# Kernel tuning notes

Measured on AMD Instinct MI355X. Metric: run time of the kernel, lower is better.

The kernel has to match this reference:

```python
import jax, jax.numpy as jnp
import numpy as np

B, CIN, COUT, H, W = 4, 128, 128, 128, 128
KH = KW = 3
KK = KH * KW
MAX_RES = 3.0


def _conv3x3(x, w, b):
    y = jax.lax.conv_general_dilated(x, w, window_strides=(1, 1), padding='SAME',
                                     dimension_numbers=('NCHW', 'OIHW', 'NCHW'))
    return y + b[None, :, None, None]


def _lrelu(x):
    return jnp.where(x >= 0, x, 0.1 * x)


def _deform_conv2d(x, offset, mask, weight, bias):
    # x: [B,C,H,W]; offset: [B,2*KK,H,W] (pairs dy,dx per tap); mask: [B,KK,H,W]
    b, c, h, w = x.shape
    cout = weight.shape[0]
    ki, kj = jnp.meshgrid(jnp.arange(KH), jnp.arange(KW), indexing='ij')
    ki = ki.reshape(KK).astype(x.dtype)
    kj = kj.reshape(KK).astype(x.dtype)
    # stride=1, padding=1, dilation=1 -> base sample position = p - 1 + k
    base_y = jnp.arange(h, dtype=x.dtype)[None, :, None] - 1.0 + ki[:, None, None]  # [KK,H,1]
    base_x = jnp.arange(w, dtype=x.dtype)[None, None, :] - 1.0 + kj[:, None, None]  # [KK,1,W]
    off = offset.reshape(b, KK, 2, h, w)
    py = base_y[None] + off[:, :, 0]  # [B,KK,H,W]
    px = base_x[None] + off[:, :, 1]
    y0 = jnp.floor(py)
    x0 = jnp.floor(px)

    def gather(img, yi, xi):  # img [C,H,W], yi/xi [KK,H,W] -> [C,KK,H,W]
        return img[:, yi, xi]

    acc = jnp.zeros((b, c, KK, h, w), dtype=x.dtype)
    for dy in (0.0, 1.0):  # 4 bilinear corners (fixed small loop)
        for dx in (0.0, 1.0):
            yc = y0 + dy
            xc = x0 + dx
            wgt = (1.0 - jnp.abs(py - yc)) * (1.0 - jnp.abs(px - xc))
            valid = (yc >= 0) & (yc <= h - 1) & (xc >= 0) & (xc <= w - 1)  # zero pad outside
            yi = jnp.clip(yc, 0, h - 1).astype(jnp.int32)
            xi = jnp.clip(xc, 0, w - 1).astype(jnp.int32)
            vals = jax.vmap(gather)(x, yi, xi)  # [B,C,KK,H,W]
            acc = acc + vals * (wgt * valid)[:, None]
    acc = acc * mask[:, None]  # modulation
    out = jnp.einsum('bckhw,ock->bohw', acc, weight.reshape(cout, c, KK))
    return out + bias[None, :, None, None]


def setup_inputs() -> dict:
    key = jax.random.key(0)
    ks = jax.random.split(key, 8)

    def he(k, shape):
        fan_in = shape[1] * shape[2] * shape[3]
        return jax.random.normal(k, shape, jnp.float32) * np.float32(np.sqrt(2.0 / fan_in))

    ccond = 2 * COUT + 2 + 1 + 2  # 261
    return {
        'x': jax.random.normal(ks[0], (B, CIN, H, W), jnp.float32),
        'cond_feat': jax.random.normal(ks[1], (B, ccond, H, W), jnp.float32),
        'flow': jax.random.normal(ks[2], (B, 2, H, W), jnp.float32),
        'w1': he(ks[3], (COUT, ccond, 3, 3)), 'b1': jnp.zeros((COUT,), jnp.float32),
        'w2': he(ks[4], (COUT, COUT, 3, 3)), 'b2': jnp.zeros((COUT,), jnp.float32),
        'w3': he(ks[5], (COUT, COUT, 3, 3)), 'b3': jnp.zeros((COUT,), jnp.float32),
        'w4': he(ks[6], (27, COUT, 3, 3)) * 0.1, 'b4': jnp.zeros((27,), jnp.float32),
        'weight': he(ks[7], (COUT, CIN, 3, 3)), 'bias': jnp.zeros((COUT,), jnp.float32),
    }


def reference(x, cond_feat, flow, w1, b1, w2, b2, w3, b3, w4, b4, weight, bias):
    f = _lrelu(_conv3x3(cond_feat, w1, b1))
    f = _lrelu(_conv3x3(f, w2, b2))
    f = _lrelu(_conv3x3(f, w3, b3))
    head = _conv3x3(f, w4, b4)  # [B, 27, H, W]
    o1, o2, m = jnp.split(head, 3, axis=1)
    offset = MAX_RES * jnp.tanh(jnp.concatenate([o1, o2], axis=1))  # [B,18,H,W]
    # flow.flip(1).repeat(1, 9, 1, 1): (fx,fy)->(fy,fx) tiled over the 9 taps
    offset = offset + jnp.tile(flow[:, ::-1], (1, KK, 1, 1))
    mask = jax.nn.sigmoid(m)  # [B,9,H,W]
    return _deform_conv2d(x, offset, mask, weight, bias)
```

## Files before the change

kernel.cpp:

```cpp
#include <hip/hip_runtime.h>
#include <cmath>

#define HH 128
#define WW 128
#define HWSZ (HH * WW)

typedef __attribute__((ext_vector_type(8))) short short8v;
typedef __attribute__((ext_vector_type(4))) float f32x4;

static __device__ __forceinline__ int imin(int a, int b) { return a < b ? a : b; }
static __device__ __forceinline__ int imax(int a, int b) { return a > b ? a : b; }

static __device__ __forceinline__ void bf16split(float f, short& hi, short& lo) {
  unsigned u = __float_as_uint(f);
  unsigned rh = u + 0x7fffu + ((u >> 16) & 1u);
  hi = (short)(rh >> 16);
  float fh = __uint_as_float((rh >> 16) << 16);
  float res = f - fh;
  unsigned v = __float_as_uint(res);
  unsigned rl = v + 0x7fffu + ((v >> 16) & 1u);
  lo = (short)(rl >> 16);
}

__global__ void wpack_kernel(const float* __restrict__ w, short* __restrict__ whi,
                             short* __restrict__ wlo, int nct, int nks,
                             int cin_real, int cout) {
  int idx = blockIdx.x * 256 + threadIdx.x;
  int total = nct * nks * 512;
  if (idx >= total) return;
  int j    = idx & 7;
  int lane = (idx >> 3) & 63;
  int t2   = idx >> 9;
  int ks   = t2 % nks;
  int ct   = t2 / nks;
  int cinb = ks / 9, tap = ks % 9;
  int cin = cinb * 32 + (lane >> 4) * 8 + j;
  int co  = ct * 16 + (lane & 15);
  float v = 0.f;
  if (co < cout && cin < cin_real) v = w[((size_t)co * cin_real + cin) * 9 + tap];
  short hi, lo;
  bf16split(v, hi, lo);
  whi[idx] = hi;
  wlo[idx] = lo;
}

template <int NCT>
__global__ __launch_bounds__(256, 2) void conv_mfma_kernel(
    const float* __restrict__ in, const short* __restrict__ wh,
    const short* __restrict__ wl, const float* __restrict__ bias,
    float* __restrict__ out, int cin_real, int CB, int cout, int lrelu) {
  __shared__ __align__(16) short s_a[3][2][66][40];

  const int tid = threadIdx.x;
  int bid = blockIdx.x;
  bid = (bid & 7) * 128 + (bid >> 3);
  const int x0 = (bid & 1) * 64;
  const int y  = (bid >> 1) & 127;
  const int b  = bid >> 8;
  const int lane = tid & 63;
  const int wv = tid >> 6;
  const int m = lane & 15;
  const int g = lane >> 4;
  const int NKS = CB * 9;

  f32x4 acc[NCT];
#pragma unroll
  for (int ct = 0; ct < NCT; ++ct) acc[ct] = (f32x4){0.f, 0.f, 0.f, 0.f};

  for (int cb = 0; cb < CB; ++cb) {
    for (int i = tid; i < 3 * 32 * 66; i += 256) {
      int px = i % 66;
      int q  = i / 66;
      int ci = q & 31;
      int row = q >> 5;
      int c  = cb * 32 + ci;
      int gy = y + row - 1;
      int gx = x0 + px - 1;
      float v = 0.f;
      if (c < cin_real && (unsigned)gy < (unsigned)HH && (unsigned)gx < (unsigned)WW)
        v = in[((size_t)(b * cin_real + c) * HH + gy) * WW + gx];
      short hi, lo;
      bf16split(v, hi, lo);
      s_a[row][0][px][ci] = hi;
      s_a[row][1][px][ci] = lo;
    }
    __syncthreads();
#pragma unroll
    for (int tap = 0; tap < 9; ++tap) {
      const int r = tap / 3;
      const int c = tap - r * 3;
      const int pxi = wv * 16 + m + c;
      short8v ah = *(const short8v*)&s_a[r][0][pxi][g * 8];
      short8v al = *(const short8v*)&s_a[r][1][pxi][g * 8];
      const int ks = cb * 9 + tap;
#pragma unroll
      for (int ct = 0; ct < NCT; ++ct) {
        const size_t off = ((size_t)(ct * NKS + ks) * 64 + lane) * 8;
        short8v bh = *(const short8v*)(wh + off);
        short8v bl = *(const short8v*)(wl + off);
        acc[ct] = __builtin_amdgcn_mfma_f32_16x16x32_bf16(ah, bh, acc[ct], 0, 0, 0);
        acc[ct] = __builtin_amdgcn_mfma_f32_16x16x32_bf16(ah, bl, acc[ct], 0, 0, 0);
        acc[ct] = __builtin_amdgcn_mfma_f32_16x16x32_bf16(al, bh, acc[ct], 0, 0, 0);
      }
    }
    __syncthreads();
  }

  const int co_l = lane & 15;
  const int pxw  = wv * 16 + (lane >> 4) * 4;
#pragma unroll
  for (int ct = 0; ct < NCT; ++ct) {
    const int co = ct * 16 + co_l;
    if (co < cout) {
      const float bv = bias[co];
      float v0 = acc[ct][0] + bv;
      float v1 = acc[ct][1] + bv;
      float v2 = acc[ct][2] + bv;
      float v3 = acc[ct][3] + bv;
      if (lrelu) {
        v0 = (v0 >= 0.f) ? v0 : 0.1f * v0;
        v1 = (v1 >= 0.f) ? v1 : 0.1f * v1;
        v2 = (v2 >= 0.f) ? v2 : 0.1f * v2;
        v3 = (v3 >= 0.f) ? v3 : 0.1f * v3;
      }
      float* op = out + ((size_t)(b * cout + co) * HH + y) * WW + x0 + pxw;
      *(float4*)op = make_float4(v0, v1, v2, v3);
    }
  }
}

__global__ __launch_bounds__(256, 2) void deform_mfma_kernel(
    const float* __restrict__ x, const float* __restrict__ head,
    const float* __restrict__ flow, const short* __restrict__ wh,
    const short* __restrict__ wl, const float* __restrict__ bias,
    float* __restrict__ out) {
  const int tid = threadIdx.x;
  int bid = blockIdx.x;
  bid = (bid & 7) * 128 + (bid >> 3);
  const int x0 = (bid & 1) * 64;
  const int y  = (bid >> 1) & 127;
  const int b  = bid >> 8;
  const int lane = tid & 63;
  const int wv = tid >> 6;
  const int m = lane & 15;
  const int g = lane >> 4;
  const int gx = x0 + wv * 16 + m;

  int   i00[9], i01[9], i10[9], i11[9];
  float w00[9], w01[9], w10[9], w11[9];
  {
    const float* hb = head + (size_t)b * 27 * HWSZ;
    const size_t pix = (size_t)y * WW + gx;
    const float fly = flow[((size_t)b * 2 + 1) * HWSZ + pix];
    const float flx = flow[((size_t)b * 2 + 0) * HWSZ + pix];
#pragma unroll
    for (int k = 0; k < 9; ++k) {
      const float hy = hb[(size_t)(2 * k) * HWSZ + pix];
      const float hx = hb[(size_t)(2 * k + 1) * HWSZ + pix];
      const float hm = hb[(size_t)(18 + k) * HWSZ + pix];
      const float dy = 3.f * tanhf(hy) + fly;
      const float dx = 3.f * tanhf(hx) + flx;
      const float py  = (float)(y - 1 + (k / 3)) + dy;
      const float pxx = (float)(gx - 1 + (k % 3)) + dx;
      const float y0f = floorf(py), x0f = floorf(pxx);
      const float fy = py - y0f, fx = pxx - x0f;
      const int iy0 = (int)y0f, ix0 = (int)x0f;
      const int iy1 = iy0 + 1,  ix1 = ix0 + 1;
      const float mm = 1.f / (1.f + expf(-hm));
      const float vy0 = (iy0 >= 0 && iy0 < HH) ? mm : 0.f;
      const float vy1 = (iy1 >= 0 && iy1 < HH) ? mm : 0.f;
      const float vx0 = (ix0 >= 0 && ix0 < WW) ? 1.f : 0.f;
      const float vx1 = (ix1 >= 0 && ix1 < WW) ? 1.f : 0.f;
      w00[k] = (1.f - fy) * (1.f - fx) * vy0 * vx0;
      w01[k] = (1.f - fy) * fx * vy0 * vx1;
      w10[k] = fy * (1.f - fx) * vy1 * vx0;
      w11[k] = fy * fx * vy1 * vx1;
      const int cy0 = imin(imax(iy0, 0), HH - 1);
      const int cy1 = imin(imax(iy1, 0), HH - 1);
      const int cx0 = imin(imax(ix0, 0), WW - 1);
      const int cx1 = imin(imax(ix1, 0), WW - 1);
      i00[k] = cy0 * WW + cx0;
      i01[k] = cy0 * WW + cx1;
      i10[k] = cy1 * WW + cx0;
      i11[k] = cy1 * WW + cx1;
    }
  }

  f32x4 acc[8];
#pragma unroll
  for (int ct = 0; ct < 8; ++ct) acc[ct] = (f32x4){0.f, 0.f, 0.f, 0.f};

  for (int cinb = 0; cinb < 4; ++cinb) {
    const float* xb = x + (size_t)(b * 128 + cinb * 32 + g * 8) * HWSZ;
#pragma unroll
    for (int tap = 0; tap < 9; ++tap) {
      float s[8];
#pragma unroll
      for (int j = 0; j < 8; ++j) {
        const float* xp = xb + (size_t)j * HWSZ;
        s[j] = w00[tap] * xp[i00[tap]] + w01[tap] * xp[i01[tap]] +
               w10[tap] * xp[i10[tap]] + w11[tap] * xp[i11[tap]];
      }
      short8v ah, al;
#pragma unroll
      for (int j = 0; j < 8; ++j) {
        short h, l;
        bf16split(s[j], h, l);
        ah[j] = h;
        al[j] = l;
      }
      const int ks = cinb * 9 + tap;
#pragma unroll
      for (int ct = 0; ct < 8; ++ct) {
        const size_t off = ((size_t)(ct * 36 + ks) * 64 + lane) * 8;
        short8v bh = *(const short8v*)(wh + off);
        short8v bl = *(const short8v*)(wl + off);
        acc[ct] = __builtin_amdgcn_mfma_f32_16x16x32_bf16(ah, bh, acc[ct], 0, 0, 0);
        acc[ct] = __builtin_amdgcn_mfma_f32_16x16x32_bf16(ah, bl, acc[ct], 0, 0, 0);
        acc[ct] = __builtin_amdgcn_mfma_f32_16x16x32_bf16(al, bh, acc[ct], 0, 0, 0);
      }
    }
  }

  const int co_l = lane & 15;
  const int pxw  = x0 + wv * 16 + (lane >> 4) * 4;
#pragma unroll
  for (int ct = 0; ct < 8; ++ct) {
    const int co = ct * 16 + co_l;
    const float bv = bias[co];
    float* op = out + ((size_t)(b * 128 + co) * HH + y) * WW + pxw;
    *(float4*)op = make_float4(acc[ct][0] + bv, acc[ct][1] + bv,
                               acc[ct][2] + bv, acc[ct][3] + bv);
  }
}

extern "C" void kernel_launch(void* const* d_in, const int* in_sizes, int n_in,
                              void* d_out, int out_size, void* d_ws, size_t ws_size,
                              hipStream_t stream) {
  const float* x    = (const float*)d_in[0];
  const float* cond = (const float*)d_in[1];
  const float* flow = (const float*)d_in[2];
  const float* w1 = (const float*)d_in[3];
  const float* b1 = (const float*)d_in[4];
  const float* w2 = (const float*)d_in[5];
  const float* b2 = (const float*)d_in[6];
  const float* w3 = (const float*)d_in[7];
  const float* b3 = (const float*)d_in[8];
  const float* w4 = (const float*)d_in[9];
  const float* b4 = (const float*)d_in[10];
  const float* wd = (const float*)d_in[11];
  const float* bd = (const float*)d_in[12];
  float* out = (float*)d_out;
  float* ws  = (float*)d_ws;

  float* f1    = ws;
  float* f2    = f1 + 8388608;
  float* headb = f2;
  short* pk1h = (short*)(f2 + 8388608);
  short* pk1l = pk1h + 331776;
  short* pk2h = pk1l + 331776;
  short* pk2l = pk2h + 147456;
  short* pk3h = pk2l + 147456;
  short* pk3l = pk3h + 147456;
  short* pk4h = pk3l + 147456;
  short* pk4l = pk4h + 36864;
  short* pkdh = pk4l + 36864;
  short* pkdl = pkdh + 147456;

  dim3 blk256(256);

  hipLaunchKernelGGL(wpack_kernel, dim3(1296), blk256, 0, stream, w1, pk1h, pk1l, 8, 81, 261, 128);
  hipLaunchKernelGGL(wpack_kernel, dim3(576),  blk256, 0, stream, w2, pk2h, pk2l, 8, 36, 128, 128);
  hipLaunchKernelGGL(wpack_kernel, dim3(576),  blk256, 0, stream, w3, pk3h, pk3l, 8, 36, 128, 128);
  hipLaunchKernelGGL(wpack_kernel, dim3(144),  blk256, 0, stream, w4, pk4h, pk4l, 2, 36, 128, 27);
  hipLaunchKernelGGL(wpack_kernel, dim3(576),  blk256, 0, stream, wd, pkdh, pkdl, 8, 36, 128, 128);

  dim3 cgrid(1024);
  hipLaunchKernelGGL(conv_mfma_kernel<8>, cgrid, blk256, 0, stream, cond, pk1h, pk1l, b1, f1, 261, 9, 128, 1);
  hipLaunchKernelGGL(conv_mfma_kernel<8>, cgrid, blk256, 0, stream, f1, pk2h, pk2l, b2, f2, 128, 4, 128, 1);
  hipLaunchKernelGGL(conv_mfma_kernel<8>, cgrid, blk256, 0, stream, f2, pk3h, pk3l, b3, f1, 128, 4, 128, 1);
  hipLaunchKernelGGL(conv_mfma_kernel<2>, cgrid, blk256, 0, stream, f1, pk4h, pk4l, b4, headb, 128, 4, 27, 0);
  hipLaunchKernelGGL(deform_mfma_kernel, cgrid, blk256, 0, stream, x, headb, flow, pkdh, pkdl, bd, out);
}
```

Measured before the change: 1.039 ms.

## Switch conv and deformable pipeline to NHWC activations with direct vector loads

Adds a transpose kernel that converts cond and x to channel-last layout, and rewrites the conv kernels to read 8 contiguous channels per tap straight from global memory instead of staging a halo tile in shared memory with barriers. Intermediate activations and the offset head are written in NHWC, so the deformable kernel's bilinear corner gathers become contiguous float4 loads instead of strided per-channel scalar loads. The costs are extra transpose passes, scattered per-element stores in the conv epilogue, and repeated global reads of the 3x3 neighbourhood that now rely on cache instead of shared-memory reuse.

After: 961.2 us. 7.5% less time.

```diff
diff --git a/kernel.cpp b/kernel.cpp
--- a/kernel.cpp
+++ b/kernel.cpp
@@ -20,6 +20,27 @@
   unsigned v = __float_as_uint(res);
   unsigned rl = v + 0x7fffu + ((v >> 16) & 1u);
   lo = (short)(rl >> 16);
+}
+
+__global__ void nhwc_kernel(const float* __restrict__ src, float* __restrict__ dst,
+                            int C_real, int CP) {
+  const int npx = 4 * HWSZ;
+  int idx = blockIdx.x * 256 + threadIdx.x;
+  int total = (CP / 8) * npx;
+  if (idx >= total) return;
+  const int pixg = idx % npx;
+  const int c8   = idx / npx;
+  const int b    = pixg / HWSZ;
+  const int pix  = pixg % HWSZ;
+  float v[8];
+#pragma unroll
+  for (int j = 0; j < 8; ++j) {
+    const int c = c8 * 8 + j;
+    v[j] = (c < C_real) ? src[((size_t)b * C_real + c) * HWSZ + pix] : 0.f;
+  }
+  float* dp = dst + (size_t)pixg * CP + c8 * 8;
+  *(float4*)dp       = make_float4(v[0], v[1], v[2], v[3]);
+  *(float4*)(dp + 4) = make_float4(v[4], v[5], v[6], v[7]);
 }
 
 __global__ void wpack_kernel(const float* __restrict__ w, short* __restrict__ whi,
@@ -45,12 +66,10 @@
 }
 
 template <int NCT>
-__global__ __launch_bounds__(256, 2) void conv_mfma_kernel(
+__global__ __launch_bounds__(256, 2) void conv_nhwc_kernel(
     const float* __restrict__ in, const short* __restrict__ wh,
     const short* __restrict__ wl, const float* __restrict__ bias,
-    float* __restrict__ out, int cin_real, int CB, int cout, int lrelu) {
-  __shared__ __align__(16) short s_a[3][2][66][40];
-
+    float* __restrict__ out, int CP, int CB, int OP, int cout, int lrelu) {
   const int tid = threadIdx.x;
   int bid = blockIdx.x;
   bid = (bid & 7) * 128 + (bid >> 3);
@@ -62,36 +81,41 @@
   const int m = lane & 15;
   const int g = lane >> 4;
   const int NKS = CB * 9;
+  const int gx = x0 + wv * 16 + m;
 
   f32x4 acc[NCT];
 #pragma unroll
   for (int ct = 0; ct < NCT; ++ct) acc[ct] = (f32x4){0.f, 0.f, 0.f, 0.f};
 
+  const float* inb = in + (size_t)b * HWSZ * CP;
+
   for (int cb = 0; cb < CB; ++cb) {
-    for (int i = tid; i < 3 * 32 * 66; i += 256) {
-      int px = i % 66;
-      int q  = i / 66;
-      int ci = q & 31;
-      int row = q >> 5;
-      int c  = cb * 32 + ci;
-      int gy = y + row - 1;
-      int gx = x0 + px - 1;
-      float v = 0.f;
-      if (c < cin_real && (unsigned)gy < (unsigned)HH && (unsigned)gx < (unsigned)WW)
-        v = in[((size_t)(b * cin_real + c) * HH + gy) * WW + gx];
-      short hi, lo;
-      bf16split(v, hi, lo);
-      s_a[row][0][px][ci] = hi;
-      s_a[row][1][px][ci] = lo;
-    }
-    __syncthreads();
+    const int cbase = cb * 32 + g * 8;
 #pragma unroll
     for (int tap = 0; tap < 9; ++tap) {
       const int r = tap / 3;
       const int c = tap - r * 3;
-      const int pxi = wv * 16 + m + c;
-      short8v ah = *(const short8v*)&s_a[r][0][pxi][g * 8];
-      short8v al = *(const short8v*)&s_a[r][1][pxi][g * 8];
+      const int gy  = y + r - 1;
+      const int gxx = gx + c - 1;
+      const bool valid = ((unsigned)gy < (unsigned)HH) && ((unsigned)gxx < (unsigned)WW);
+      const int cy = imin(imax(gy, 0), HH - 1);
+      const int cx = imin(imax(gxx, 0), WW - 1);
+      const float* ap = inb + (size_t)(cy * WW + cx) * CP + cbase;
+      f32x4 a0 = *(const f32x4*)ap;
+      f32x4 a1 = *(const f32x4*)(ap + 4);
+      if (!valid) {
+        a0 = (f32x4){0.f, 0.f, 0.f, 0.f};
+        a1 = (f32x4){0.f, 0.f, 0.f, 0.f};
+      }
+      short8v ah, al;
+#pragma unroll
+      for (int j = 0; j < 4; ++j) {
+        short h, l;
+        bf16split(a0[j], h, l);
+        ah[j] = h; al[j] = l;
+        bf16split(a1[j], h, l);
+        ah[j + 4] = h; al[j + 4] = l;
+      }
       const int ks = cb * 9 + tap;
 #pragma unroll
       for (int ct = 0; ct < NCT; ++ct) {
@@ -103,34 +127,27 @@
         acc[ct] = __builtin_amdgcn_mfma_f32_16x16x32_bf16(al, bh, acc[ct], 0, 0, 0);
       }
     }
-    __syncthreads();
   }
 
   const int co_l = lane & 15;
-  const int pxw  = wv * 16 + (lane >> 4) * 4;
+  const int px0  = x0 + wv * 16 + (lane >> 4) * 4;
 #pragma unroll
   for (int ct = 0; ct < NCT; ++ct) {
     const int co = ct * 16 + co_l;
     if (co < cout) {
       const float bv = bias[co];
-      float v0 = acc[ct][0] + bv;
-      float v1 = acc[ct][1] + bv;
-      float v2 = acc[ct][2] + bv;
-      float v3 = acc[ct][3] + bv;
-      if (lrelu) {
-        v0 = (v0 >= 0.f) ? v0 : 0.1f * v0;
-        v1 = (v1 >= 0.f) ? v1 : 0.1f * v1;
-        v2 = (v2 >= 0.f) ? v2 : 0.1f * v2;
-        v3 = (v3 >= 0.f) ? v3 : 0.1f * v3;
-      }
-      float* op = out + ((size_t)(b * cout + co) * HH + y) * WW + x0 + pxw;
-      *(float4*)op = make_float4(v0, v1, v2, v3);
+#pragma unroll
+      for (int q = 0; q < 4; ++q) {
+        float v = acc[ct][q] + bv;
+        if (lrelu) v = (v >= 0.f) ? v : 0.1f * v;
+        out[((size_t)b * HWSZ + y * WW + px0 + q) * OP + co] = v;
+      }
     }
   }
 }
 
-__global__ __launch_bounds__(256, 2) void deform_mfma_kernel(
-    const float* __restrict__ x, const float* __restrict__ head,
+__global__ __launch_bounds__(256, 2) void deform_nhwc_kernel(
+    const float* __restrict__ xt, const float* __restrict__ headt,
     const float* __restrict__ flow, const short* __restrict__ wh,
     const short* __restrict__ wl, const float* __restrict__ bias,
     float* __restrict__ out) {
@@ -149,15 +166,15 @@
   int   i00[9], i01[9], i10[9], i11[9];
   float w00[9], w01[9], w10[9], w11[9];
   {
-    const float* hb = head + (size_t)b * 27 * HWSZ;
     const size_t pix = (size_t)y * WW + gx;
+    const float* hb = headt + ((size_t)b * HWSZ + pix) * 32;
     const float fly = flow[((size_t)b * 2 + 1) * HWSZ + pix];
     const float flx = flow[((size_t)b * 2 + 0) * HWSZ + pix];
 #pragma unroll
     for (int k = 0; k < 9; ++k) {
-      const float hy = hb[(size_t)(2 * k) * HWSZ + pix];
-      const float hx = hb[(size_t)(2 * k + 1) * HWSZ + pix];
-      const float hm = hb[(size_t)(18 + k) * HWSZ + pix];
+      const float hy = hb[2 * k];
+      const float hx = hb[2 * k + 1];
+      const float hm = hb[18 + k];
       const float dy = 3.f * tanhf(hy) + fly;
       const float dx = 3.f * tanhf(hx) + flx;
       const float py  = (float)(y - 1 + (k / 3)) + dy;
@@ -190,24 +207,32 @@
 #pragma unroll
   for (int ct = 0; ct < 8; ++ct) acc[ct] = (f32x4){0.f, 0.f, 0.f, 0.f};
 
+  const float* xb = xt + (size_t)b * HWSZ * 128;
+
   for (int cinb = 0; cinb < 4; ++cinb) {
-    const float* xb = x + (size_t)(b * 128 + cinb * 32 + g * 8) * HWSZ;
+    const int cbase = cinb * 32 + g * 8;
 #pragma unroll
     for (int tap = 0; tap < 9; ++tap) {
-      float s[8];
-#pragma unroll
-      for (int j = 0; j < 8; ++j) {
-        const float* xp = xb + (size_t)j * HWSZ;
-        s[j] = w00[tap] * xp[i00[tap]] + w01[tap] * xp[i01[tap]] +
-               w10[tap] * xp[i10[tap]] + w11[tap] * xp[i11[tap]];
-      }
+      const float* p00 = xb + (size_t)i00[tap] * 128 + cbase;
+      const float* p01 = xb + (size_t)i01[tap] * 128 + cbase;
+      const float* p10 = xb + (size_t)i10[tap] * 128 + cbase;
+      const float* p11 = xb + (size_t)i11[tap] * 128 + cbase;
+      f32x4 c00a = *(const f32x4*)p00, c00b = *(const f32x4*)(p00 + 4);
+      f32x4 c01a = *(const f32x4*)p01, c01b = *(const f32x4*)(p01 + 4);
+      f32x4 c10a = *(const f32x4*)p10, c10b = *(const f32x4*)(p10 + 4);
+      f32x4 c11a = *(const f32x4*)p11, c11b = *(const f32x4*)(p11 + 4);
       short8v ah, al;
 #pragma unroll
-      for (int j = 0; j < 8; ++j) {
+      for (int j = 0; j < 4; ++j) {
+        float s0 = w00[tap] * c00a[j] + w01[tap] * c01a[j] +
+                   w10[tap] * c10a[j] + w11[tap] * c11a[j];
+        float s1 = w00[tap] * c00b[j] + w01[tap] * c01b[j] +
+                   w10[tap] * c10b[j] + w11[tap] * c11b[j];
         short h, l;
-        bf16split(s[j], h, l);
-        ah[j] = h;
-        al[j] = l;
+        bf16split(s0, h, l);
+        ah[j] = h; al[j] = l;
+        bf16split(s1, h, l);
+        ah[j + 4] = h; al[j + 4] = l;
       }
       const int ks = cinb * 9 + tap;
 #pragma unroll
@@ -253,10 +278,13 @@
   float* out = (float*)d_out;
   float* ws  = (float*)d_ws;
 
-  float* f1    = ws;
-  float* f2    = f1 + 8388608;
-  float* headb = f2;
-  short* pk1h = (short*)(f2 + 8388608);
+  float* A  = ws;
+  float* condt = A;
+  float* f2    = A;
+  float* headt = A;
+  float* xt    = A + 8388608;
+  float* f1    = ws + 18874368;
+  short* pk1h = (short*)(ws + 27262976);
   short* pk1l = pk1h + 331776;
   short* pk2h = pk1l + 331776;
   short* pk2l = pk2h + 147456;
@@ -269,6 +297,7 @@
 
   dim3 blk256(256);
 
+  hipLaunchKernelGGL(nhwc_kernel, dim3(9216), blk256, 0, stream, cond, condt, 261, 288);
   hipLaunchKernelGGL(wpack_kernel, dim3(1296), blk256, 0, stream, w1, pk1h, pk1l, 8, 81, 261, 128);
   hipLaunchKernelGGL(wpack_kernel, dim3(576),  blk256, 0, stream, w2, pk2h, pk2l, 8, 36, 128, 128);
   hipLaunchKernelGGL(wpack_kernel, dim3(576),  blk256, 0, stream, w3, pk3h, pk3l, 8, 36, 128, 128);
@@ -276,9 +305,10 @@
   hipLaunchKernelGGL(wpack_kernel, dim3(576),  blk256, 0, stream, wd, pkdh, pkdl, 8, 36, 128, 128);
 
   dim3 cgrid(1024);
-  hipLaunchKernelGGL(conv_mfma_kernel<8>, cgrid, blk256, 0, stream, cond, pk1h, pk1l, b1, f1, 261, 9, 128, 1);
-  hipLaunchKernelGGL(conv_mfma_kernel<8>, cgrid, blk256, 0, stream, f1, pk2h, pk2l, b2, f2, 128, 4, 128, 1);
-  hipLaunchKernelGGL(conv_mfma_kernel<8>, cgrid, blk256, 0, stream, f2, pk3h, pk3l, b3, f1, 128, 4, 128, 1);
-  hipLaunchKernelGGL(conv_mfma_kernel<2>, cgrid, blk256, 0, stream, f1, pk4h, pk4l, b4, headb, 128, 4, 27, 0);
-  hipLaunchKernelGGL(deform_mfma_kernel, cgrid, blk256, 0, stream, x, headb, flow, pkdh, pkdl, bd, out);
-}
+  hipLaunchKernelGGL(conv_nhwc_kernel<8>, cgrid, blk256, 0, stream, condt, pk1h, pk1l, b1, f1, 288, 9, 128, 128, 1);
+  hipLaunchKernelGGL(nhwc_kernel, dim3(4096), blk256, 0, stream, x, xt, 128, 128);
+  hipLaunchKernelGGL(conv_nhwc_kernel<8>, cgrid, blk256, 0, stream, f1, pk2h, pk2l, b2, f2, 128, 4, 128, 128, 1);
+  hipLaunchKernelGGL(conv_nhwc_kernel<8>, cgrid, blk256, 0, stream, f2, pk3h, pk3l, b3, f1, 128, 4, 128, 128, 1);
+  hipLaunchKernelGGL(conv_nhwc_kernel<2>, cgrid, blk256, 0, stream, f1, pk4h, pk4l, b4, headt, 128, 4, 32, 27, 0);
+  hipLaunchKernelGGL(deform_nhwc_kernel, cgrid, blk256, 0, stream, xt, headt, flow, pkdh, pkdl, bd, out);
+}
```
